# Performance work log

Measured on AMD Instinct MI355X. Metric: run time of the kernel, lower is better.

The kernel has to match this reference:

```python
import jax, jax.numpy as jnp
import numpy as np


def graph_conv(x, W, b, src, dst, n_nodes):
    """DGL GraphConv, norm='both', activation=relu.
    Pre-scale by out-degree^-1/2 of src, project (in>out so project first),
    sum-aggregate over edges, post-scale by in-degree^-1/2 of dst."""
    ones = jnp.ones(src.shape[0], dtype=x.dtype)
    deg_out = jax.ops.segment_sum(ones, src, num_segments=n_nodes)
    deg_in = jax.ops.segment_sum(ones, dst, num_segments=n_nodes)
    norm_src = jnp.clip(deg_out, 1.0, None) ** -0.5  # [N]
    norm_dst = jnp.clip(deg_in, 1.0, None) ** -0.5   # [N]
    h = x * norm_src[:, None]
    h = h @ W  # project first since in_feats > out_feats
    # message passing: gather src features, scatter-add into dst
    agg = jax.ops.segment_sum(h[src], dst, num_segments=n_nodes)  # [N, out]
    agg = agg * norm_dst[:, None]
    return jax.nn.relu(agg + b)


def setup_inputs() -> dict:
    key = jax.random.key(0)
    ks = jax.random.split(key, 6)
    N, E, D_IN, D_HID = 50000, 800000, 1024, 256
    x = jax.random.normal(ks[0], (N, D_IN), dtype=jnp.float32)
    src = jax.random.randint(ks[1], (E,), 0, N)
    dst = jax.random.randint(ks[2], (E,), 0, N)
    # Glorot-style init for weights
    W1 = jax.random.normal(ks[3], (D_IN, D_HID), dtype=jnp.float32) * (1.0 / np.sqrt(D_IN))
    b1 = jnp.zeros((D_HID,), dtype=jnp.float32)
    W2 = jax.random.normal(ks[4], (D_HID, 1), dtype=jnp.float32) * (1.0 / np.sqrt(D_HID))
    b2 = jnp.zeros((1,), dtype=jnp.float32)
    return {"x": x, "src": src, "dst": dst, "W1": W1, "b1": b1, "W2": W2, "b2": b2, "n_nodes": N}


def reference(x, src, dst, W1, b1, W2, b2, n_nodes):
    h = graph_conv(x, W1, b1, src, dst, n_nodes)   # [N, 256]
    out = graph_conv(h, W2, b2, src, dst, n_nodes)  # [N, 1]
    return out
```

## Files before the change

kernel.cpp:

```cpp
#include <hip/hip_runtime.h>
#include <hip/hip_bf16.h>

typedef __attribute__((ext_vector_type(8))) short bf16x8;
typedef __attribute__((ext_vector_type(4))) float f32x4;

static __device__ __forceinline__ short f2bf(float f) {
    unsigned u = __float_as_uint(f);
    unsigned r = (u + 0x7FFFu + ((u >> 16) & 1u)) >> 16;
    return (short)(unsigned short)r;
}
static __device__ __forceinline__ float bf2f(short s) {
    return __uint_as_float(((unsigned)(unsigned short)s) << 16);
}

static __device__ __forceinline__ void gload16(const void* g, void* l) {
    __builtin_amdgcn_global_load_lds((const __attribute__((address_space(1))) unsigned int*)g,
                                     (__attribute__((address_space(3))) unsigned int*)l, 16, 0, 0);
}

static __device__ __forceinline__ void wg_barrier() {
    asm volatile("" ::: "memory");
    __builtin_amdgcn_s_barrier();
    asm volatile("" ::: "memory");
}

static __device__ __forceinline__ bf16x8 cvt8(const f32x4 lo, const f32x4 hi) {
    __hip_bfloat162 p0 = __float22bfloat162_rn(make_float2(lo[0], lo[1]));
    __hip_bfloat162 p1 = __float22bfloat162_rn(make_float2(lo[2], lo[3]));
    __hip_bfloat162 p2 = __float22bfloat162_rn(make_float2(hi[0], hi[1]));
    __hip_bfloat162 p3 = __float22bfloat162_rn(make_float2(hi[2], hi[3]));
    short2 s0 = *(short2*)&p0, s1 = *(short2*)&p1, s2 = *(short2*)&p2, s3 = *(short2*)&p3;
    bf16x8 r = {s0.x, s0.y, s1.x, s1.y, s2.x, s2.y, s3.x, s3.y};
    return r;
}

__global__ void deg_kernel(const int* __restrict__ src, const int* __restrict__ dst,
                           int* __restrict__ deg_out, int* __restrict__ deg_in, int E) {
    int e = blockIdx.x * blockDim.x + threadIdx.x;
    if (e < E) {
        atomicAdd(&deg_out[src[e]], 1);
        atomicAdd(&deg_in[dst[e]], 1);
    }
}

__global__ void scan_part1(const int* __restrict__ deg, int* __restrict__ bsum, int N) {
    __shared__ int red[256];
    int i = blockIdx.x * 256 + threadIdx.x;
    red[threadIdx.x] = (i < N) ? deg[i] : 0;
    __syncthreads();
    for (int off = 128; off > 0; off >>= 1) {
        if (threadIdx.x < off) red[threadIdx.x] += red[threadIdx.x + off];
        __syncthreads();
    }
    if (threadIdx.x == 0) bsum[blockIdx.x] = red[0];
}

__global__ void scan_part2(const int* __restrict__ bsum, int* __restrict__ bsum_ex, int NB,
                           int* __restrict__ offsets, int N, int E) {
    __shared__ int s[256];
    int t = threadIdx.x;
    int v = (t < NB) ? bsum[t] : 0;
    s[t] = v;
    __syncthreads();
    for (int off = 1; off < 256; off <<= 1) {
        int u = (t >= off) ? s[t - off] : 0;
        __syncthreads();
        s[t] += u;
        __syncthreads();
    }
    bsum_ex[t] = s[t] - v;
    if (t == 0) offsets[N] = E;
}

__global__ void scan_part3(const int* __restrict__ deg_in, const int* __restrict__ deg_out,
                           const int* __restrict__ bsum_ex, int* __restrict__ offsets,
                           float* __restrict__ ns, float* __restrict__ nd, int N) {
    __shared__ int s[256];
    int t = threadIdx.x, i = blockIdx.x * 256 + t;
    int v = (i < N) ? deg_in[i] : 0;
    s[t] = v;
    __syncthreads();
    for (int off = 1; off < 256; off <<= 1) {
        int u = (t >= off) ? s[t - off] : 0;
        __syncthreads();
        s[t] += u;
        __syncthreads();
    }
    if (i < N) {
        offsets[i] = bsum_ex[blockIdx.x] + s[t] - v;
        ns[i] = rsqrtf((float)max(deg_out[i], 1));
        nd[i] = rsqrtf((float)max(v, 1));
    }
}

__global__ void scatter_kernel(const int* __restrict__ src, const int* __restrict__ dst,
                               const int* __restrict__ offsets, int* __restrict__ cursor,
                               int* __restrict__ bucket, int E) {
    int e = blockIdx.x * blockDim.x + threadIdx.x;
    if (e < E) {
        int d = dst[e];
        int p = atomicAdd(&cursor[d], 1);
        bucket[offsets[d] + p] = src[e];
    }
}

__global__ __launch_bounds__(1024) void transpose_w1(const float* __restrict__ W1,
                                                     short* __restrict__ Wt) {
    __shared__ short tile[32][33];
    int k0 = blockIdx.x * 32, n0 = blockIdx.y * 32;
    int tx = threadIdx.x & 31, ty = threadIdx.x >> 5;
    tile[ty][tx] = f2bf(W1[(size_t)(k0 + ty) * 256 + (n0 + tx)]);
    __syncthreads();
    Wt[(size_t)(n0 + ty) * 1024 + (k0 + tx)] = tile[tx][ty];
}

#define BM 128
#define BN 256
#define BK 32
#define NKT 32
#define CSTR 264

union SMem {
    struct {
        float A[2][BM * BK];
        short B[2][BN * BK];
    } s;
    short C[BM * CSTR];
};

__global__ __launch_bounds__(256, 2) void gemm1_kernel(const float* __restrict__ x,
                                                       const short* __restrict__ Wt,
                                                       const float* __restrict__ norm_src,
                                                       short* __restrict__ hb, int M) {
    __shared__ __align__(16) SMem sm;
    __shared__ float ns_lds[BM];
    const int tid  = threadIdx.x;
    const int lane = tid & 63;
    const int wave = tid >> 6;
    const int quad = lane >> 4;
    const int mrow = lane & 15;
    const int wm = (wave >> 1) * 64;
    const int wn = (wave & 1) * 128;
    const int bm = blockIdx.x * BM;

    if (tid < BM) ns_lds[tid] = norm_src[min(bm + tid, M - 1)];

    f32x4 acc[4][8] = {};

    const int aL_r = lane >> 3;
    const int aL_c = (lane & 7) ^ (aL_r & 7);
    const int bL_r = lane >> 2;
    const int bL_c = (lane & 3) ^ ((lane >> 3) & 3);

    auto stageAB = [&](int buf, int k0) {
#pragma unroll
        for (int i = 0; i < 4; i++) {
            int rowbase = wave * 32 + i * 8;
            int r = min(bm + rowbase + aL_r, M - 1);
            gload16(x + (size_t)r * 1024 + k0 + aL_c * 4, &sm.s.A[buf][rowbase * 32]);
        }
#pragma unroll
        for (int i = 0; i < 4; i++) {
            int nbase = wave * 64 + i * 16;
            int n = nbase + bL_r;
            gload16(Wt + (size_t)n * 1024 + k0 + bL_c * 8, &sm.s.B[buf][nbase * 32]);
        }
    };

    stageAB(0, 0);
    stageAB(1, BK);
    asm volatile("s_waitcnt vmcnt(8)" ::: "memory");
    wg_barrier();

    int cur = 0;
    for (int t = 0; t < NKT; t++) {
        bf16x8 af[4], bfr[8];
#pragma unroll
        for (int mi = 0; mi < 4; mi++) {
            int row = wm + mi * 16 + mrow;
            f32x4 lo = *(const f32x4*)&sm.s.A[cur][row * 32 + (((quad * 2 + 0) ^ (mrow & 7)) * 4)];
            f32x4 hi = *(const f32x4*)&sm.s.A[cur][row * 32 + (((quad * 2 + 1) ^ (mrow & 7)) * 4)];
            af[mi] = cvt8(lo, hi);
        }
#pragma unroll
        for (int ni = 0; ni < 8; ni++) {
            int n = wn + ni * 16 + mrow;
            bfr[ni] = *(const bf16x8*)&sm.s.B[cur][n * 32 + ((quad ^ ((mrow >> 1) & 3)) * 8)];
        }
#pragma unroll
        for (int mi = 0; mi < 4; mi++)
#pragma unroll
            for (int ni = 0; ni < 8; ni++)
                acc[mi][ni] = __builtin_amdgcn_mfma_f32_16x16x32_bf16(af[mi], bfr[ni], acc[mi][ni], 0, 0, 0);

        wg_barrier();

        if (t + 2 < NKT) {
            stageAB(cur, (t + 2) * BK);
            asm volatile("s_waitcnt vmcnt(8)" ::: "memory");
        } else {
            asm volatile("s_waitcnt vmcnt(0)" ::: "memory");
        }
        wg_barrier();
        cur ^= 1;
    }

#pragma unroll
    for (int mi = 0; mi < 4; mi++) {
#pragma unroll
        for (int reg = 0; reg < 4; reg++) {
            int row = wm + mi * 16 + quad * 4 + reg;
            float nsv = ns_lds[row];
#pragma unroll
            for (int ni = 0; ni < 8; ni++) {
                int col = wn + ni * 16 + mrow;
                sm.C[row * CSTR + col] = f2bf(acc[mi][ni][reg] * nsv);
            }
        }
    }
    __syncthreads();
#pragma unroll
    for (int j = 0; j < 16; j++) {
        int row = wave * 2 + (lane >> 5) + j * 8;
        int chunk = lane & 31;
        if (bm + row < M) {
            int4 v = *(const int4*)&sm.C[row * CSTR + chunk * 8];
            *(int4*)(hb + (size_t)(bm + row) * 256 + chunk * 8) = v;
        }
    }
}

__global__ __launch_bounds__(256) void agg1_kernel(const short* __restrict__ hb,
                                                   const int* __restrict__ bucket,
                                                   const int* __restrict__ offsets,
                                                   const float* __restrict__ norm_dst,
                                                   const float* __restrict__ norm_src,
                                                   const float* __restrict__ b1,
                                                   const float* __restrict__ W2,
                                                   float* __restrict__ z, int N) {
    int wave = threadIdx.x >> 6;
    int lane = threadIdx.x & 63;
    int half = lane >> 5;
    int col8 = lane & 31;
    int node = blockIdx.x * 4 + wave;
    if (node >= N) return;
    int beg = offsets[node], end = offsets[node + 1];
    float a[8] = {0.f, 0.f, 0.f, 0.f, 0.f, 0.f, 0.f, 0.f};
    int e = beg;
    for (; e + 8 <= end; e += 8) {
        int s0 = bucket[e + 0 + half];
        int s1 = bucket[e + 2 + half];
        int s2 = bucket[e + 4 + half];
        int s3 = bucket[e + 6 + half];
        bf16x8 v0 = *(const bf16x8*)(hb + (size_t)s0 * 256 + col8 * 8);
        bf16x8 v1 = *(const bf16x8*)(hb + (size_t)s1 * 256 + col8 * 8);
        bf16x8 v2 = *(const bf16x8*)(hb + (size_t)s2 * 256 + col8 * 8);
        bf16x8 v3 = *(const bf16x8*)(hb + (size_t)s3 * 256 + col8 * 8);
#pragma unroll
        for (int j = 0; j < 8; j++)
            a[j] += bf2f(v0[j]) + bf2f(v1[j]) + bf2f(v2[j]) + bf2f(v3[j]);
    }
    for (; e + 2 <= end; e += 2) {
        int s0 = bucket[e + half];
        bf16x8 v0 = *(const bf16x8*)(hb + (size_t)s0 * 256 + col8 * 8);
#pragma unroll
        for (int j = 0; j < 8; j++) a[j] += bf2f(v0[j]);
    }
    if (e < end && half == 0) {
        int s0 = bucket[e];
        bf16x8 v0 = *(const bf16x8*)(hb + (size_t)s0 * 256 + col8 * 8);
#pragma unroll
        for (int j = 0; j < 8; j++) a[j] += bf2f(v0[j]);
    }
#pragma unroll
    for (int j = 0; j < 8; j++) a[j] += __shfl_xor(a[j], 32, 64);

    float nd = norm_dst[node];
    float4 b_lo = *(const float4*)(b1 + col8 * 8);
    float4 b_hi = *(const float4*)(b1 + col8 * 8 + 4);
    float4 w_lo = *(const float4*)(W2 + col8 * 8);
    float4 w_hi = *(const float4*)(W2 + col8 * 8 + 4);
    float p = 0.f;
    p += fmaxf(a[0] * nd + b_lo.x, 0.f) * w_lo.x;
    p += fmaxf(a[1] * nd + b_lo.y, 0.f) * w_lo.y;
    p += fmaxf(a[2] * nd + b_lo.z, 0.f) * w_lo.z;
    p += fmaxf(a[3] * nd + b_lo.w, 0.f) * w_lo.w;
    p += fmaxf(a[4] * nd + b_hi.x, 0.f) * w_hi.x;
    p += fmaxf(a[5] * nd + b_hi.y, 0.f) * w_hi.y;
    p += fmaxf(a[6] * nd + b_hi.z, 0.f) * w_hi.z;
    p += fmaxf(a[7] * nd + b_hi.w, 0.f) * w_hi.w;
#pragma unroll
    for (int off = 16; off > 0; off >>= 1) p += __shfl_xor(p, off, 64);
    if (lane == 0) z[node] = p * norm_src[node];
}

__global__ void agg2_kernel(const float* __restrict__ z, const int* __restrict__ bucket,
                            const int* __restrict__ offsets, const float* __restrict__ norm_dst,
                            const float* __restrict__ b2, float* __restrict__ out, int N) {
    int i = blockIdx.x * blockDim.x + threadIdx.x;
    if (i >= N) return;
    int beg = offsets[i], end = offsets[i + 1];
    float s = 0.f;
    for (int e = beg; e < end; e++) s += z[bucket[e]];
    out[i] = fmaxf(s * norm_dst[i] + b2[0], 0.f);
}

extern "C" void kernel_launch(void* const* d_in, const int* in_sizes, int n_in,
                              void* d_out, int out_size, void* d_ws, size_t ws_size,
                              hipStream_t stream) {
    const int D_HID = in_sizes[4];
    const int D_IN  = in_sizes[3] / D_HID;
    const int N     = in_sizes[0] / D_IN;
    const int E     = in_sizes[1];

    const float* x   = (const float*)d_in[0];
    const int*   src = (const int*)d_in[1];
    const int*   dst = (const int*)d_in[2];
    const float* W1  = (const float*)d_in[3];
    const float* b1  = (const float*)d_in[4];
    const float* W2  = (const float*)d_in[5];
    const float* b2  = (const float*)d_in[6];
    float* out = (float*)d_out;

    char* p = (char*)d_ws;
    auto alloc = [&](size_t bytes) {
        void* r = (void*)p;
        p += (bytes + 255) & ~(size_t)255;
        return r;
    };
    int*   deg_out  = (int*)alloc((size_t)N * 4);
    int*   deg_in   = (int*)alloc((size_t)N * 4);
    int*   cursor   = (int*)alloc((size_t)N * 4);
    float* norm_src = (float*)alloc((size_t)N * 4);
    float* norm_dst = (float*)alloc((size_t)N * 4);
    int*   offsets  = (int*)alloc((size_t)(N + 1) * 4);
    int*   bucket   = (int*)alloc((size_t)E * 4);
    short* Wt       = (short*)alloc((size_t)D_IN * D_HID * 2);
    short* hb       = (short*)alloc((size_t)N * D_HID * 2);
    float* z        = (float*)alloc((size_t)N * 4);
    int*   bsum     = (int*)alloc(256 * 4);
    int*   bsum_ex  = (int*)alloc(256 * 4);

    const int NB = (N + 255) / 256;

    size_t degpad = ((size_t)N * 4 + 255) & ~(size_t)255;
    hipMemsetAsync(deg_out, 0, degpad * 2 + (size_t)N * 4, stream);

    deg_kernel<<<(E + 255) / 256, 256, 0, stream>>>(src, dst, deg_out, deg_in, E);
    scan_part1<<<NB, 256, 0, stream>>>(deg_in, bsum, N);
    scan_part2<<<1, 256, 0, stream>>>(bsum, bsum_ex, NB, offsets, N, E);
    scan_part3<<<NB, 256, 0, stream>>>(deg_in, deg_out, bsum_ex, offsets, norm_src, norm_dst, N);
    scatter_kernel<<<(E + 255) / 256, 256, 0, stream>>>(src, dst, offsets, cursor, bucket, E);
    transpose_w1<<<dim3(D_IN / 32, D_HID / 32), 1024, 0, stream>>>(W1, Wt);
    gemm1_kernel<<<dim3((N + BM - 1) / BM), 256, 0, stream>>>(x, Wt, norm_src, hb, N);
    agg1_kernel<<<(N + 3) / 4, 256, 0, stream>>>(hb, bucket, offsets, norm_dst, norm_src, b1, W2, z, N);
    agg2_kernel<<<(N + 255) / 256, 256, 0, stream>>>(z, bucket, offsets, norm_dst, b2, out, N);
}
```

Before: 488.5 us.

## Load GEMM A operand directly into registers with one-step prefetch, bypassing LDS

The fp32 x tiles are no longer staged through shared memory. Each lane now reads its own MFMA fragment rows from global memory into registers one k-step ahead and converts them to bf16 after the barrier. Only the bf16 weight tile stays double-buffered in LDS. This removes the LDS write/read round trip and the bank-swizzle reads for A. In exchange, the two waves that share the same rows each fetch them from global memory, relying on L2 to absorb the duplication, and register pressure goes up.

```diff
diff --git a/kernel.cpp b/kernel.cpp
--- a/kernel.cpp
+++ b/kernel.cpp
@@ -121,10 +121,7 @@
 #define CSTR 264
 
 union SMem {
-    struct {
-        float A[2][BM * BK];
-        short B[2][BN * BK];
-    } s;
+    short B[2][BN * BK];
     short C[BM * CSTR];
 };
 
@@ -147,45 +144,56 @@
 
     f32x4 acc[4][8] = {};
 
-    const int aL_r = lane >> 3;
-    const int aL_c = (lane & 7) ^ (aL_r & 7);
+    const float* aptr[4];
+#pragma unroll
+    for (int mi = 0; mi < 4; mi++) {
+        int row = min(bm + wm + mi * 16 + mrow, M - 1);
+        aptr[mi] = x + (size_t)row * 1024 + quad * 8;
+    }
+
     const int bL_r = lane >> 2;
     const int bL_c = (lane & 3) ^ ((lane >> 3) & 3);
 
-    auto stageAB = [&](int buf, int k0) {
-#pragma unroll
-        for (int i = 0; i < 4; i++) {
-            int rowbase = wave * 32 + i * 8;
-            int r = min(bm + rowbase + aL_r, M - 1);
-            gload16(x + (size_t)r * 1024 + k0 + aL_c * 4, &sm.s.A[buf][rowbase * 32]);
-        }
+    auto stageB = [&](int buf, int k0) {
 #pragma unroll
         for (int i = 0; i < 4; i++) {
             int nbase = wave * 64 + i * 16;
             int n = nbase + bL_r;
-            gload16(Wt + (size_t)n * 1024 + k0 + bL_c * 8, &sm.s.B[buf][nbase * 32]);
+            gload16(Wt + (size_t)n * 1024 + k0 + bL_c * 8, &sm.B[buf][nbase * 32]);
         }
     };
 
-    stageAB(0, 0);
-    stageAB(1, BK);
-    asm volatile("s_waitcnt vmcnt(8)" ::: "memory");
+    f32x4 aLo[4], aHi[4];
+    bf16x8 af[4];
+
+    stageB(0, 0);
+#pragma unroll
+    for (int mi = 0; mi < 4; mi++) {
+        aLo[mi] = *(const f32x4*)(aptr[mi]);
+        aHi[mi] = *(const f32x4*)(aptr[mi] + 4);
+    }
+    stageB(1, BK);
+    asm volatile("s_waitcnt vmcnt(4)" ::: "memory");
+#pragma unroll
+    for (int mi = 0; mi < 4; mi++) af[mi] = cvt8(aLo[mi], aHi[mi]);
     wg_barrier();
 
     int cur = 0;
     for (int t = 0; t < NKT; t++) {
-        bf16x8 af[4], bfr[8];
-#pragma unroll
-        for (int mi = 0; mi < 4; mi++) {
-            int row = wm + mi * 16 + mrow;
-            f32x4 lo = *(const f32x4*)&sm.s.A[cur][row * 32 + (((quad * 2 + 0) ^ (mrow & 7)) * 4)];
-            f32x4 hi = *(const f32x4*)&sm.s.A[cur][row * 32 + (((quad * 2 + 1) ^ (mrow & 7)) * 4)];
-            af[mi] = cvt8(lo, hi);
-        }
+        if (t + 1 < NKT) {
+            int k = (t + 1) * BK;
+#pragma unroll
+            for (int mi = 0; mi < 4; mi++) {
+                aLo[mi] = *(const f32x4*)(aptr[mi] + k);
+                aHi[mi] = *(const f32x4*)(aptr[mi] + k + 4);
+            }
+        }
+
+        bf16x8 bfr[8];
 #pragma unroll
         for (int ni = 0; ni < 8; ni++) {
             int n = wn + ni * 16 + mrow;
-            bfr[ni] = *(const bf16x8*)&sm.s.B[cur][n * 32 + ((quad ^ ((mrow >> 1) & 3)) * 8)];
+            bfr[ni] = *(const bf16x8*)&sm.B[cur][n * 32 + ((quad ^ ((mrow >> 1) & 3)) * 8)];
         }
 #pragma unroll
         for (int mi = 0; mi < 4; mi++)
@@ -196,10 +204,14 @@
         wg_barrier();
 
         if (t + 2 < NKT) {
-            stageAB(cur, (t + 2) * BK);
-            asm volatile("s_waitcnt vmcnt(8)" ::: "memory");
+            stageB(cur, (t + 2) * BK);
+            asm volatile("s_waitcnt vmcnt(4)" ::: "memory");
         } else {
             asm volatile("s_waitcnt vmcnt(0)" ::: "memory");
+        }
+        if (t + 1 < NKT) {
+#pragma unroll
+            for (int mi = 0; mi < 4; mi++) af[mi] = cvt8(aLo[mi], aHi[mi]);
         }
         wg_barrier();
         cur ^= 1;
```

New measurement: 512.6 us. +4.9%, slower.
